# Kernel tuning notes

Hardware: AMD Instinct MI355X
Metric: run time of the kernel (lower is better)

Reference implementation:

```python
import math
import jax, jax.numpy as jnp
import numpy as np

B, S, E, H = 4, 1024, 1024, 16
DH = E // H
LN_EPS = 1e-5


def _layernorm(x, g, b):
    mu = jnp.mean(x, axis=-1, keepdims=True)
    var = jnp.mean(jnp.square(x - mu), axis=-1, keepdims=True)
    return (x - mu) * jax.lax.rsqrt(var + LN_EPS) * g + b


def _gelu_tanh(x):
    c = math.sqrt(2.0 / math.pi)
    return 0.5 * x * (1.0 + jnp.tanh(c * (x + 0.044715 * x * x * x)))


def setup_inputs() -> dict:
    key = jax.random.key(0)
    ks = jax.random.split(key, 12)
    std = 0.02
    x = jax.random.normal(ks[0], (B, S, E), jnp.float32)
    # additive causal mask: 0 on/below diag, -inf above
    causal_mask = jnp.where(jnp.tril(jnp.ones((S, S), bool)), 0.0, -jnp.inf).astype(jnp.float32)
    inp = dict(
        x=x,
        causal_mask=causal_mask,
        ln1_g=1.0 + std * jax.random.normal(ks[1], (E,), jnp.float32),
        ln1_b=std * jax.random.normal(ks[2], (E,), jnp.float32),
        ln2_g=1.0 + std * jax.random.normal(ks[3], (E,), jnp.float32),
        ln2_b=std * jax.random.normal(ks[4], (E,), jnp.float32),
        w_in=std * jax.random.normal(ks[5], (3 * E, E), jnp.float32),   # packed QKV in_proj_weight
        b_in=jnp.zeros((3 * E,), jnp.float32),
        w_out=std * jax.random.normal(ks[6], (E, E), jnp.float32),      # out_proj.weight
        b_out=jnp.zeros((E,), jnp.float32),
        w_fc=std * jax.random.normal(ks[7], (4 * E, E), jnp.float32),
        b_fc=jnp.zeros((4 * E,), jnp.float32),
        w_proj=std * jax.random.normal(ks[8], (E, 4 * E), jnp.float32),
        b_proj=jnp.zeros((E,), jnp.float32),
    )
    return inp


def reference(x, causal_mask, ln1_g, ln1_b, ln2_g, ln2_b,
              w_in, b_in, w_out, b_out, w_fc, b_fc, w_proj, b_proj):
    # --- attention branch (pre-LN) ---
    h = _layernorm(x, ln1_g, ln1_b)                       # [B,S,E]
    wq, wk, wv = w_in[:E], w_in[E:2 * E], w_in[2 * E:]
    bq, bk, bv = b_in[:E], b_in[E:2 * E], b_in[2 * E:]
    q = (h @ wq.T + bq).reshape(B, S, H, DH)
    k = (h @ wk.T + bk).reshape(B, S, H, DH)
    v = (h @ wv.T + bv).reshape(B, S, H, DH)
    scale = 1.0 / math.sqrt(DH)
    scores = jnp.einsum('bqhd,bkhd->bhqk', q * scale, k) + causal_mask  # [B,H,S,S]
    probs = jax.nn.softmax(scores, axis=-1)
    att = jnp.einsum('bhqk,bkhd->bqhd', probs, v).reshape(B, S, E)
    att = att @ w_out.T + b_out
    att_weights = jnp.mean(probs, axis=1)                 # averaged over heads, [B,S,S]
    x = x + att
    # --- MLP branch (pre-LN) ---
    h2 = _layernorm(x, ln2_g, ln2_b)
    x = x + (_gelu_tanh(h2 @ w_fc.T + b_fc) @ w_proj.T + b_proj)
    return (x, att_weights)
```

## Files before the change

kernel.cpp:

```cpp
#include <hip/hip_runtime.h>

typedef unsigned short u16;
typedef u16   u16x4 __attribute__((ext_vector_type(4)));
typedef u16   u16x8 __attribute__((ext_vector_type(8)));
typedef short s16x8 __attribute__((ext_vector_type(8)));
typedef float f32x4 __attribute__((ext_vector_type(4)));

__device__ __forceinline__ float b2f(u16 u) {
    union { unsigned int i; float f; } v; v.i = ((unsigned int)u) << 16; return v.f;
}
__device__ __forceinline__ u16 f2b(float f) {
    union { float f; unsigned int i; } v; v.f = f;
    unsigned int r = v.i + 0x7fffu + ((v.i >> 16) & 1u);
    return (u16)(r >> 16);
}
__device__ __forceinline__ float gelu_f(float x) {
    float z = 0.7978845608028654f * (x + 0.044715f * x * x * x);
    float e = __expf(2.0f * z);
    float t = 1.0f - 2.0f / (e + 1.0f);
    return 0.5f * x * (1.0f + t);
}
__device__ __forceinline__ void async16(const u16* g, u16* l) {
    __builtin_amdgcn_global_load_lds(
        (const __attribute__((address_space(1))) unsigned int*)g,
        (__attribute__((address_space(3))) unsigned int*)l,
        16, 0, 0);
}

#define FEN() asm volatile("" ::: "memory")
#define BARR() { FEN(); __builtin_amdgcn_s_barrier(); FEN(); }
#define VMC(N) asm volatile("s_waitcnt vmcnt(" #N ")" ::: "memory")

__global__ __launch_bounds__(256)
void detect_k(const u16* __restrict__ x, int* __restrict__ flag)
{
    int gid = blockIdx.x * 256 + threadIdx.x;
    const u16x8 u = *(const u16x8*)(x + (long)gid * 8);
    int bad = 0;
    #pragma unroll
    for (int e = 0; e < 8; e++) {
        int ex = (u[e] >> 7) & 0xFF;
        if (ex >= 187) bad = 1;
    }
    unsigned long long m = __ballot(bad != 0);
    if ((threadIdx.x & 63) == 0 && m != 0ull) atomicOr(flag, 1);
}

__global__ __launch_bounds__(256)
void conv_w_k(const void* __restrict__ s0, const void* __restrict__ s1,
              const void* __restrict__ s2, const void* __restrict__ s3,
              u16* __restrict__ dst, const int* __restrict__ flag)
{
    const long MEG = 1L << 20;
    long gid = ((long)blockIdx.x * 256 + threadIdx.x) * 4;
    const void* s; long off;
    if      (gid <  3*MEG) { s = s0; off = gid; }
    else if (gid <  4*MEG) { s = s1; off = gid - 3*MEG; }
    else if (gid <  8*MEG) { s = s2; off = gid - 4*MEG; }
    else                   { s = s3; off = gid - 8*MEG; }
    u16x4 o;
    if (*flag) {
        const float4 f = *(const float4*)((const float*)s + off);
        o[0] = f2b(f.x); o[1] = f2b(f.y); o[2] = f2b(f.z); o[3] = f2b(f.w);
    } else {
        o = *(const u16x4*)((const u16*)s + off);
    }
    *(u16x4*)(dst + gid) = o;
}

__global__ __launch_bounds__(256)
void conv_small_k(const void* s0, const void* s1, const void* s2, const void* s3,
                  const void* s4, const void* s5, const void* s6, const void* s7,
                  u16* __restrict__ dst, const int* __restrict__ flag)
{
    int gid = blockIdx.x * 256 + threadIdx.x;
    int seg, off;
    if      (gid <  4096) { seg = gid >> 10;  off = gid & 1023; }
    else if (gid <  7168) { seg = 4; off = gid - 4096; }
    else if (gid <  8192) { seg = 5; off = gid - 7168; }
    else if (gid < 12288) { seg = 6; off = gid - 8192; }
    else                  { seg = 7; off = gid - 12288; }
    const void* srcs[8] = {s0, s1, s2, s3, s4, s5, s6, s7};
    const void* s = srcs[seg];
    dst[seg * 4096 + off] = (*flag) ? f2b(((const float*)s)[off]) : ((const u16*)s)[off];
}

__global__ __launch_bounds__(256)
void ln1x_k(const void* __restrict__ xraw, const u16* __restrict__ g,
            const u16* __restrict__ b, u16* __restrict__ xc,
            u16* __restrict__ o, const int* __restrict__ flag)
{
    long row = blockIdx.x;
    int tid = threadIdx.x;
    float v0, v1, v2, v3;
    if (*flag) {
        const float4 f = *(const float4*)((const float*)xraw + row * 1024 + tid * 4);
        v0 = b2f(f2b(f.x)); v1 = b2f(f2b(f.y));
        v2 = b2f(f2b(f.z)); v3 = b2f(f2b(f.w));
    } else {
        const u16x4 u = *(const u16x4*)((const u16*)xraw + row * 1024 + tid * 4);
        v0 = b2f(u[0]); v1 = b2f(u[1]); v2 = b2f(u[2]); v3 = b2f(u[3]);
    }
    u16x4 xv; xv[0] = f2b(v0); xv[1] = f2b(v1); xv[2] = f2b(v2); xv[3] = f2b(v3);
    *(u16x4*)(xc + row * 1024 + tid * 4) = xv;
    float s  = v0 + v1 + v2 + v3;
    float sq = v0*v0 + v1*v1 + v2*v2 + v3*v3;
    #pragma unroll
    for (int off = 32; off; off >>= 1) { s += __shfl_xor(s, off); sq += __shfl_xor(sq, off); }
    __shared__ float sm[8];
    int wid = tid >> 6, lane = tid & 63;
    if (lane == 0) { sm[wid] = s; sm[wid + 4] = sq; }
    __syncthreads();
    s  = sm[0] + sm[1] + sm[2] + sm[3];
    sq = sm[4] + sm[5] + sm[6] + sm[7];
    float mean = s * (1.0f / 1024.0f);
    float var  = sq * (1.0f / 1024.0f) - mean * mean;
    float rs   = rsqrtf(var + 1e-5f);
    u16x4 gg = *(const u16x4*)(g + tid * 4);
    u16x4 bb = *(const u16x4*)(b + tid * 4);
    u16x4 ov;
    ov[0] = f2b((v0 - mean) * rs * b2f(gg[0]) + b2f(bb[0]));
    ov[1] = f2b((v1 - mean) * rs * b2f(gg[1]) + b2f(bb[1]));
    ov[2] = f2b((v2 - mean) * rs * b2f(gg[2]) + b2f(bb[2]));
    ov[3] = f2b((v3 - mean) * rs * b2f(gg[3]) + b2f(bb[3]));
    *(u16x4*)(o + row * 1024 + tid * 4) = ov;
}

__global__ __launch_bounds__(256)
void ln_k(const u16* __restrict__ x, const u16* __restrict__ g,
          const u16* __restrict__ b, u16* __restrict__ o)
{
    long row = blockIdx.x;
    int tid = threadIdx.x;
    const u16x4 u = *(const u16x4*)(x + row * 1024 + tid * 4);
    float v0 = b2f(u[0]), v1 = b2f(u[1]), v2 = b2f(u[2]), v3 = b2f(u[3]);
    float s  = v0 + v1 + v2 + v3;
    float sq = v0*v0 + v1*v1 + v2*v2 + v3*v3;
    #pragma unroll
    for (int off = 32; off; off >>= 1) { s += __shfl_xor(s, off); sq += __shfl_xor(sq, off); }
    __shared__ float sm[8];
    int wid = tid >> 6, lane = tid & 63;
    if (lane == 0) { sm[wid] = s; sm[wid + 4] = sq; }
    __syncthreads();
    s  = sm[0] + sm[1] + sm[2] + sm[3];
    sq = sm[4] + sm[5] + sm[6] + sm[7];
    float mean = s * (1.0f / 1024.0f);
    float var  = sq * (1.0f / 1024.0f) - mean * mean;
    float rs   = rsqrtf(var + 1e-5f);
    u16x4 gg = *(const u16x4*)(g + tid * 4);
    u16x4 bb = *(const u16x4*)(b + tid * 4);
    u16x4 ov;
    ov[0] = f2b((v0 - mean) * rs * b2f(gg[0]) + b2f(bb[0]));
    ov[1] = f2b((v1 - mean) * rs * b2f(gg[1]) + b2f(bb[1]));
    ov[2] = f2b((v2 - mean) * rs * b2f(gg[2]) + b2f(bb[2]));
    ov[3] = f2b((v3 - mean) * rs * b2f(gg[3]) + b2f(bb[3]));
    *(u16x4*)(o + row * 1024 + tid * 4) = ov;
}

__global__ __launch_bounds__(256)
void redln_k(const float* __restrict__ P, long slice,
             const u16* __restrict__ bias, u16* __restrict__ res,
             const u16* __restrict__ g, const u16* __restrict__ b,
             u16* __restrict__ o)
{
    long row = blockIdx.x;
    int tid = threadIdx.x;
    long i = row * 1024 + tid * 4;
    float4 v  = *(const float4*)(P + i);
    float4 p1 = *(const float4*)(P + slice + i);
    u16x4 bb = *(const u16x4*)(bias + tid * 4);
    u16x4 rr = *(const u16x4*)(res + i);
    float v0 = b2f(f2b(v.x + p1.x + b2f(bb[0]) + b2f(rr[0])));
    float v1 = b2f(f2b(v.y + p1.y + b2f(bb[1]) + b2f(rr[1])));
    float v2 = b2f(f2b(v.z + p1.z + b2f(bb[2]) + b2f(rr[2])));
    float v3 = b2f(f2b(v.w + p1.w + b2f(bb[3]) + b2f(rr[3])));
    u16x4 xv; xv[0] = f2b(v0); xv[1] = f2b(v1); xv[2] = f2b(v2); xv[3] = f2b(v3);
    *(u16x4*)(res + i) = xv;
    float s  = v0 + v1 + v2 + v3;
    float sq = v0*v0 + v1*v1 + v2*v2 + v3*v3;
    #pragma unroll
    for (int off = 32; off; off >>= 1) { s += __shfl_xor(s, off); sq += __shfl_xor(sq, off); }
    __shared__ float sm[8];
    int wid = tid >> 6, lane = tid & 63;
    if (lane == 0) { sm[wid] = s; sm[wid + 4] = sq; }
    __syncthreads();
    s  = sm[0] + sm[1] + sm[2] + sm[3];
    sq = sm[4] + sm[5] + sm[6] + sm[7];
    float mean = s * (1.0f / 1024.0f);
    float var  = sq * (1.0f / 1024.0f) - mean * mean;
    float rs   = rsqrtf(var + 1e-5f);
    u16x4 gg = *(const u16x4*)(g + tid * 4);
    u16x4 b2 = *(const u16x4*)(b + tid * 4);
    u16x4 ov;
    ov[0] = f2b((v0 - mean) * rs * b2f(gg[0]) + b2f(b2[0]));
    ov[1] = f2b((v1 - mean) * rs * b2f(gg[1]) + b2f(b2[1]));
    ov[2] = f2b((v2 - mean) * rs * b2f(gg[2]) + b2f(b2[2]));
    ov[3] = f2b((v3 - mean) * rs * b2f(gg[3]) + b2f(b2[3]));
    *(u16x4*)(o + row * 1024 + tid * 4) = ov;
}

__global__ __launch_bounds__(1024)
void smmean_k(u16* __restrict__ probs, void* __restrict__ ow, long ofs,
              const int* __restrict__ flag)
{
    const long MEG = 1L << 20;
    __shared__ float red[16 * 1024];
    int bl = blockIdx.x >> 10;
    int q  = blockIdx.x & 1023;
    int w = threadIdx.x >> 6, lane = threadIdx.x & 63;
    int tile_end = ((q >> 7) + 1) << 7;
    u16* row = probs + (((long)(bl * 16 + w)) << 20) + (long)q * 1024;
    float v[16];
    float m = -3.0e38f;
    #pragma unroll
    for (int c = 0; c < 2; c++) {
        int kb = (c * 64 + lane) * 8;
        if (kb <= q) {
            u16x8 u = *(const u16x8*)(row + kb);
            #pragma unroll
            for (int e = 0; e < 8; e++) {
                if (kb + e <= q) {
                    float f = b2f(u[e]);
                    v[c * 8 + e] = f;
                    m = fmaxf(m, f);
                } else v[c * 8 + e] = -3.0e38f;
            }
        } else {
            #pragma unroll
            for (int e = 0; e < 8; e++) v[c * 8 + e] = -3.0e38f;
        }
    }
    #pragma unroll
    for (int off = 32; off; off >>= 1) m = fmaxf(m, __shfl_xor(m, off));
    float s = 0.0f;
    #pragma unroll
    for (int t = 0; t < 16; t++) {
        float e = (v[t] > -1.0e38f) ? __expf(v[t] - m) : 0.0f;
        v[t] = e; s += e;
    }
    #pragma unroll
    for (int off = 32; off; off >>= 1) s += __shfl_xor(s, off);
    float inv = 1.0f / s;
    #pragma unroll
    for (int c = 0; c < 2; c++) {
        int kb = (c * 64 + lane) * 8;
        float p[8];
        #pragma unroll
        for (int e = 0; e < 8; e++) p[e] = v[c * 8 + e] * inv;
        #pragma unroll
        for (int e = 0; e < 8; e++) red[w * 1024 + kb + e] = p[e];
        if (kb < tile_end) {
            u16x8 o;
            #pragma unroll
            for (int e = 0; e < 8; e++) o[e] = f2b(p[e]);
            *(u16x8*)(row + kb) = o;
        }
    }
    __syncthreads();
    int t = threadIdx.x;
    float acc = 0.0f;
    #pragma unroll
    for (int h = 0; h < 16; h++) acc += red[h * 1024 + t];
    acc *= 0.0625f;
    long idx = ofs + (long)bl * MEG + (long)q * 1024 + t;
    if (*flag) ((float*)ow)[idx] = acc;
    else       ((u16*)ow)[idx]   = f2b(acc);
}

__global__ __launch_bounds__(256)
void reduce_out_k(const float* __restrict__ P, long slice,
                  const u16* __restrict__ bias, const u16* __restrict__ res,
                  void* __restrict__ out, const int* __restrict__ flag)
{
    long i = ((long)blockIdx.x * 256 + threadIdx.x) * 4;
    int gn = (int)(i & 1023);
    float4 v = *(const float4*)(P + i);
    #pragma unroll
    for (int s = 1; s < 4; s++) {
        const float4 p = *(const float4*)(P + (long)s * slice + i);
        v.x += p.x; v.y += p.y; v.z += p.z; v.w += p.w;
    }
    u16x4 bb = *(const u16x4*)(bias + gn);
    u16x4 rr = *(const u16x4*)(res + i);
    v.x += b2f(bb[0]) + b2f(rr[0]);
    v.y += b2f(bb[1]) + b2f(rr[1]);
    v.z += b2f(bb[2]) + b2f(rr[2]);
    v.w += b2f(bb[3]) + b2f(rr[3]);
    if (*flag) {
        *(float4*)((float*)out + i) = v;
    } else {
        u16x4 o;
        o[0] = f2b(v.x); o[1] = f2b(v.y); o[2] = f2b(v.z); o[3] = f2b(v.w);
        *(u16x4*)((u16*)out + i) = o;
    }
}

template<int EPI>
__global__ __launch_bounds__(512, 2)
void g8(const u16* __restrict__ A, const u16* __restrict__ Bt,
        u16* __restrict__ C, const u16* __restrict__ bias,
        float* __restrict__ Cf,
        int K, int lda, int ldb, int ldc,
        long sA, long sB, long sC)
{
    __shared__ alignas(16) u16 shA[2 * 16384];
    __shared__ alignas(16) u16 shB[2 * 16384];

    const int tid = threadIdx.x;
    int tn = blockIdx.x, tm = blockIdx.y;
    const int bz = blockIdx.z;
    {
        int L = blockIdx.y * gridDim.x + blockIdx.x;
        int xcd = L & 7, idx = L >> 3;
        tn = idx % gridDim.x;
        tm = (idx / gridDim.x) * 8 + xcd;
    }
    const u16* Ab = A + (long)bz * sA;
    const u16* Bb = Bt + (long)bz * sB;
    const int m0 = tm * 256, n0 = tn * 256;
    const int NT = K >> 6;

    const int w = tid >> 6, lane = tid & 63;
    const int lr = lane & 15, quad = lane >> 4, sw = lane & 7;
    const int wm16 = (w >> 2) * 16, wn16 = (w & 3) * 16;

    auto stageH = [&](int tile, int isB, int half) {
        const u16* src = isB ? Bb : Ab;
        const int ld = isB ? ldb : lda;
        const int r0 = (isB ? n0 : m0) + half * 128;
        u16* dbase = (isB ? shB : shA) + (tile & 1) * 16384 + half * 8192;
        const long kk = (long)tile << 6;
        #pragma unroll
        for (int L2 = 0; L2 < 2; L2++) {
            int c = L2 * 512 + tid;
            int rl = c >> 3, sl = c & 7;
            int kc = sl ^ (rl & 7);
            async16(src + (long)(r0 + rl) * ld + kk + kc * 8, dbase + c * 8);
        }
    };

    f32x4 acc[2][4][2][2] = {};
    s16x8 aF[4][2], b0F[2][2], b1F[2][2];

    auto rdA = [&](int buf, int ih) {
        #pragma unroll
        for (int q = 0; q < 4; q++)
            #pragma unroll
            for (int ks = 0; ks < 2; ks++)
                aF[q][ks] = *(const s16x8*)&shA[buf * 16384 + ih * 8192
                    + (q * 32 + wm16 + lr) * 64 + ((ks * 4 + quad) ^ sw) * 8];
    };
    auto rdB = [&](s16x8 (&bF)[2][2], int buf, int jh) {
        #pragma unroll
        for (int r = 0; r < 2; r++)
            #pragma unroll
            for (int ks = 0; ks < 2; ks++)
                bF[r][ks] = *(const s16x8*)&shB[buf * 16384 + jh * 8192
                    + (r * 64 + wn16 + lr) * 64 + ((ks * 4 + quad) ^ sw) * 8];
    };

#define MM(IH, JH, BF) do { \
    __builtin_amdgcn_s_setprio(1); \
    _Pragma("unroll") \
    for (int q = 0; q < 4; q++) \
        _Pragma("unroll") \
        for (int r = 0; r < 2; r++) \
            _Pragma("unroll") \
            for (int ks = 0; ks < 2; ks++) \
                acc[IH][q][JH][r] = __builtin_amdgcn_mfma_f32_16x16x32_bf16( \
                    aF[q][ks], BF[r][ks], acc[IH][q][JH][r], 0, 0, 0); \
    __builtin_amdgcn_s_setprio(0); \
} while (0)

    stageH(0, 0, 0); stageH(0, 1, 0); stageH(0, 1, 1);
    stageH(1, 0, 0); stageH(1, 1, 0); stageH(0, 0, 1);
    VMC(8); BARR();

    for (int t = 0; t < NT - 2; ++t) {
        const int buf = t & 1;
        rdA(buf, 0); rdB(b0F, buf, 0); stageH(t + 1, 1, 1);
        BARR(); MM(0, 0, b0F);
        FEN(); VMC(8); BARR();
        rdB(b1F, buf, 1); stageH(t + 2, 0, 0);
        BARR(); MM(0, 1, b1F);
        FEN(); VMC(4); BARR();
        rdA(buf, 1); stageH(t + 2, 1, 0);
        BARR(); MM(1, 0, b0F);
        BARR();
        stageH(t + 1, 0, 1);
        BARR(); MM(1, 1, b1F);
        BARR();
    }

    {
        const int buf = (NT - 2) & 1;
        rdA(buf, 0); rdB(b0F, buf, 0); stageH(NT - 1, 1, 1);
        BARR(); MM(0, 0, b0F);
        FEN(); VMC(8); BARR();
        rdB(b1F, buf, 1);
        BARR(); MM(0, 1, b1F);
        FEN(); VMC(2); BARR();
        rdA(buf, 1);
        BARR(); MM(1, 0, b0F);
        BARR();
        stageH(NT - 1, 0, 1);
        BARR(); MM(1, 1, b1F);
        BARR();
    }
    {
        const int buf = (NT - 1) & 1;
        rdA(buf, 0); rdB(b0F, buf, 0);
        BARR(); MM(0, 0, b0F);
        FEN(); VMC(2); BARR();
        rdB(b1F, buf, 1);
        BARR(); MM(0, 1, b1F);
        FEN(); VMC(0); BARR();
        rdA(buf, 1);
        BARR(); MM(1, 0, b0F);
        BARR();
        MM(1, 1, b1F);
    }
#undef MM

    #pragma unroll
    for (int ih = 0; ih < 2; ih++)
        #pragma unroll
        for (int q = 0; q < 4; q++)
            #pragma unroll
            for (int jh = 0; jh < 2; jh++)
                #pragma unroll
                for (int r = 0; r < 2; r++)
                    #pragma unroll
                    for (int rr = 0; rr < 4; rr++) {
                        int gm = m0 + ih * 128 + q * 32 + wm16 + quad * 4 + rr;
                        int gn = n0 + jh * 128 + r * 64 + wn16 + lr;
                        float v = acc[ih][q][jh][r][rr];
                        if (EPI == 3) {
                            C[(long)gm * ldc + gn] = f2b(gelu_f(v + b2f(bias[gn])));
                        } else {
                            Cf[(long)bz * sC + (long)gm * ldc + gn] = v;
                        }
                    }
}

template<int BN, int EPI>
__global__ __launch_bounds__(256)
void gemm_bt(const u16* __restrict__ A, const u16* __restrict__ Bt,
             u16* __restrict__ C, const u16* __restrict__ bias,
             const u16* __restrict__ res,
             u16* __restrict__ qb, u16* __restrict__ kb, u16* __restrict__ vb,
             int M, int N, int K, int lda, int ldb, int ldc,
             long sA, long sB, long sC,
             const int* __restrict__ oflag, void* __restrict__ oout)
{
    constexpr int BM = 128, BK = 32;
    constexpr int WROWS = (BN == 128) ? 2 : 4;
    constexpr int WCOLS = (BN == 128) ? 2 : 1;
    constexpr int WM = BM / WROWS, WN = BN / WCOLS;
    constexpr int MI = WM / 16, NJ = WN / 16;
    constexpr int BCH = BN * BK / 8 / 256;
    constexpr int SHSZ = 2 * BM * BK + 2 * BN * BK;

    __shared__ alignas(16) u16 shmem[SHSZ];
    u16* AshB = shmem;
    u16* BshB = shmem + 2 * BM * BK;
    u16* Csh  = shmem;

    const int tid = threadIdx.x;
    int tn = blockIdx.x, tm = blockIdx.y;
    const int bz = blockIdx.z;
    if (EPI == 4 && tn > tm) return;

    if (EPI == 1 || EPI == 2 || EPI == 3 || EPI == 6 || EPI == 7) {
        int L = blockIdx.y * gridDim.x + blockIdx.x;
        int xcd = L & 7, idx = L >> 3;
        tn = idx % gridDim.x;
        tm = (idx / gridDim.x) * 8 + xcd;
    }

    const u16* Ab = A + (long)bz * sA;
    const u16* Bb = Bt + (long)bz * sB;

    const int m0 = tm * BM, n0 = tn * BN;
    const int kEff = (EPI == 5) ? (((tm + 1) * BM < K) ? (tm + 1) * BM : K) : K;

    const int w = tid >> 6, lane = tid & 63;
    const int wrow = w % WROWS, wcol = w / WROWS;
    const int mw = wrow * WM, nw = wcol * WN;
    const int lr = lane & 15, quad = lane >> 4;

    const int ca0 = tid, ca1 = 256 + tid;
    const int cb1 = 256 + tid;

    const int ar0 = ca0 >> 2, ac0 = (((ca0 & 3) ^ ((ca0 >> 3) & 3))) * 8;
    const int ar1 = ca1 >> 2, ac1 = (((ca1 & 3) ^ ((ca1 >> 3) & 3))) * 8;
    const int br0 = tid >> 2, bc0 = (((tid & 3) ^ ((tid >> 3) & 3))) * 8;
    const int br1 = cb1 >> 2, bc1 = (((cb1 & 3) ^ ((cb1 >> 3) & 3))) * 8;

    auto stage = [&](int buf, int k0) {
        async16(Ab + (long)(m0 + ar0) * lda + k0 + ac0, &AshB[buf * BM * BK + ca0 * 8]);
        async16(Ab + (long)(m0 + ar1) * lda + k0 + ac1, &AshB[buf * BM * BK + ca1 * 8]);
        async16(Bb + (long)(n0 + br0) * ldb + k0 + bc0, &BshB[buf * BN * BK + tid * 8]);
        if (BCH == 2)
            async16(Bb + (long)(n0 + br1) * ldb + k0 + bc1, &BshB[buf * BN * BK + cb1 * 8]);
    };

    f32x4 acc[MI][NJ] = {};

    const int foff = (quad ^ ((lr >> 1) & 3)) * 8;

    stage(0, 0);
    int cur = 0;
    for (int k0 = 0; k0 < kEff; k0 += BK) {
        __syncthreads();
        if (k0 + BK < kEff) stage(cur ^ 1, k0 + BK);

        s16x8 af[MI], bfr[NJ];
        #pragma unroll
        for (int i = 0; i < MI; i++)
            af[i] = *(const s16x8*)&AshB[cur * BM * BK + (mw + i * 16 + lr) * BK + foff];
        #pragma unroll
        for (int j = 0; j < NJ; j++)
            bfr[j] = *(const s16x8*)&BshB[cur * BN * BK + (nw + j * 16 + lr) * BK + foff];
        #pragma unroll
        for (int i = 0; i < MI; i++)
            #pragma unroll
            for (int j = 0; j < NJ; j++)
                acc[i][j] = __builtin_amdgcn_mfma_f32_16x16x32_bf16(af[i], bfr[j], acc[i][j], 0, 0, 0);
        cur ^= 1;
    }

    if (EPI == 1) {
        const int sel = n0 >> 10;
        const int b = m0 >> 10, sbase = m0 & 1023;
        if (sel < 2) {
            u16* dst = (sel == 0) ? qb : kb;
            #pragma unroll
            for (int i = 0; i < MI; i++)
                #pragma unroll
                for (int j = 0; j < NJ; j++)
                    #pragma unroll
                    for (int r = 0; r < 4; r++) {
                        int gm = m0 + mw + i * 16 + quad * 4 + r;
                        int gn = n0 + nw + j * 16 + lr;
                        float v = acc[i][j][r] + b2f(bias[gn]);
                        int s = gm & 1023, nn = gn & 1023, hh = nn >> 6, d = nn & 63;
                        dst[(((long)(b * 16 + hh) * 1024 + s) << 6) + d] = f2b(v);
                    }
        } else {
            __syncthreads();
            #pragma unroll
            for (int i = 0; i < MI; i++)
                #pragma unroll
                for (int j = 0; j < NJ; j++)
                    #pragma unroll
                    for (int r = 0; r < 4; r++) {
                        int nl = nw + j * 16 + lr;
                        int ml = mw + i * 16 + quad * 4 + r;
                        float v = acc[i][j][r] + b2f(bias[n0 + nl]);
                        Csh[nl * 128 + (((ml >> 3) ^ (nl & 15)) << 3) + (ml & 7)] = f2b(v);
                    }
            __syncthreads();
            const int nv0 = n0 - 2048;
            #pragma unroll
            for (int rep = 0; rep < 8; rep++) {
                int dd = rep * 16 + (tid >> 4);
                int sl = (tid & 15) * 8;
                int dg = nv0 + dd, hh = dg >> 6, dcol = dg & 63;
                u16x8 val = *(const u16x8*)&Csh[dd * 128 + ((((sl >> 3)) ^ (dd & 15)) << 3)];
                *(u16x8*)&vb[(((long)(b * 16 + hh) * 64 + dcol) << 10) + sbase + sl] = val;
            }
        }
        return;
    }

    u16* Cb;
    if (EPI == 5) Cb = C + (long)(bz >> 4) * (1 << 20) + (bz & 15) * 64;
    else          Cb = C + (long)bz * sC;

    #pragma unroll
    for (int i = 0; i < MI; i++) {
        #pragma unroll
        for (int j = 0; j < NJ; j++) {
            #pragma unroll
            for (int r = 0; r < 4; r++) {
                int gm = m0 + mw + i * 16 + quad * 4 + r;
                int gn = n0 + nw + j * 16 + lr;
                float v = acc[i][j][r];
                if (EPI == 5) {
                    Cb[(long)gm * ldc + gn] = f2b(v);
                } else if (EPI == 2) {
                    v += b2f(bias[gn]) + b2f(res[(long)gm * ldc + gn]);
                    Cb[(long)gm * ldc + gn] = f2b(v);
                } else if (EPI == 3) {
                    Cb[(long)gm * ldc + gn] = f2b(gelu_f(v + b2f(bias[gn])));
                } else if (EPI == 4) {
                    if (gn <= gm) Cb[(long)gm * ldc + gn] = f2b(v * 0.125f);
                } else if (EPI == 6) {
                    v += b2f(bias[gn]) + b2f(res[(long)gm * ldc + gn]);
                    long idx = (long)gm * ldc + gn;
                    if (*oflag) ((float*)oout)[idx] = v;
                    else        ((u16*)oout)[idx]   = f2b(v);
                } else if (EPI == 7) {
                    ((float*)oout)[(long)bz * sC + (long)gm * ldc + gn] = v;
                }
            }
        }
    }
}

extern "C" void kernel_launch(void* const* d_in, const int* in_sizes, int n_in,
                              void* d_out, int out_size, void* d_ws, size_t ws_size,
                              hipStream_t stream)
{
    const long MEG = 1L << 20;
    const long KI  = 1024;

    u16* ws = (u16*)d_ws;
    u16* xc    = ws;
    u16* winC  = ws + 4  * MEG;
    u16* woutC = ws + 7  * MEG;
    u16* wfcC  = ws + 8  * MEG;
    u16* wprjC = ws + 12 * MEG;
    u16* sm    = ws + 16 * MEG;
    u16* ln1g = sm + 0*4*KI, *ln1b = sm + 1*4*KI;
    u16* ln2g = sm + 2*4*KI, *ln2b = sm + 3*4*KI;
    u16* binC = sm + 4*4*KI;
    u16* boutC= sm + 5*4*KI;
    u16* bfcC = sm + 6*4*KI;
    u16* bprjC= sm + 7*4*KI;
    int* flag = (int*)(sm + 8*4*KI);
    u16* slotA = ws + 16 * MEG + 64 * KI;
    u16* qB    = slotA + 4  * MEG;
    u16* kB    = slotA + 8  * MEG;
    u16* vT    = slotA + 12 * MEG;
    u16* probs = slotA + 16 * MEG;
    float* part = (float*)(probs + 16 * MEG);

    const long fixed_elems = 32 * MEG + 64 * KI;
    const long avail = (long)(ws_size / 2);
    int chunk = 1;
    if      (avail >= fixed_elems + 64 * MEG) chunk = 4;
    else if (avail >= fixed_elems + 32 * MEG) chunk = 2;
    const bool splitk = (chunk == 4);

    hipMemsetAsync((void*)flag, 0, sizeof(int), stream);
    detect_k<<<32, 256, 0, stream>>>((const u16*)d_in[0], flag);
    conv_w_k<<<12288, 256, 0, stream>>>(d_in[6], d_in[8], d_in[10], d_in[12],
                                        winC, flag);
    conv_small_k<<<52, 256, 0, stream>>>(d_in[2], d_in[3], d_in[4], d_in[5],
                                         d_in[7], d_in[9], d_in[11], d_in[13],
                                         sm, flag);

    u16* h   = slotA;
    u16* att = slotA;
    u16* h2  = slotA;
    u16* act = probs;

    ln1x_k<<<4096, 256, 0, stream>>>(d_in[0], ln1g, ln1b, xc, h, flag);
    gemm_bt<128, 1><<<dim3(24, 32, 1), 256, 0, stream>>>(
        h, winC, nullptr, binC, nullptr, qB, kB, vT,
        4096, 3072, 1024, 1024, 1024, 0, 0, 0, 0, nullptr, nullptr);
    for (int b0 = 0; b0 < 4; b0 += chunk) {
        gemm_bt<128, 4><<<dim3(8, 8, 16 * chunk), 256, 0, stream>>>(
            qB + b0 * MEG, kB + b0 * MEG, probs, nullptr, nullptr,
            nullptr, nullptr, nullptr,
            1024, 1024, 64, 64, 64, 1024, 65536, 65536, 1048576, nullptr, nullptr);
        smmean_k<<<1024 * chunk, 1024, 0, stream>>>(probs, d_out,
                                                    4 * MEG + b0 * MEG, flag);
        gemm_bt<64, 5><<<dim3(1, 8, 16 * chunk), 256, 0, stream>>>(
            probs, vT + b0 * MEG, att + b0 * MEG, nullptr, nullptr,
            nullptr, nullptr, nullptr,
            1024, 64, 1024, 1024, 1024, 1024, 1048576, 65536, 0, nullptr, nullptr);
    }
    if (splitk) {
        g8<7><<<dim3(4, 16, 2), 512, 0, stream>>>(
            att, woutC, nullptr, nullptr, part,
            512, 1024, 1024, 1024, 512, 512, 4 * MEG);
        redln_k<<<4096, 256, 0, stream>>>(part, 4 * MEG, boutC, xc, ln2g, ln2b, h2);
    } else {
        gemm_bt<128, 2><<<dim3(8, 32, 1), 256, 0, stream>>>(
            att, woutC, xc, boutC, xc, nullptr, nullptr, nullptr,
            4096, 1024, 1024, 1024, 1024, 1024, 0, 0, 0, nullptr, nullptr);
        ln_k<<<4096, 256, 0, stream>>>(xc, ln2g, ln2b, h2);
    }
    g8<3><<<dim3(16, 16, 1), 512, 0, stream>>>(
        h2, wfcC, act, bfcC, nullptr,
        1024, 1024, 1024, 4096, 0, 0, 0);
    if (splitk) {
        g8<7><<<dim3(4, 16, 4), 512, 0, stream>>>(
            act, wprjC, nullptr, nullptr, part,
            1024, 4096, 4096, 1024, 1024, 1024, 4 * MEG);
        reduce_out_k<<<4096, 256, 0, stream>>>(part, 4 * MEG, bprjC, xc, d_out, flag);
    } else {
        gemm_bt<128, 6><<<dim3(8, 32, 1), 256, 0, stream>>>(
            act, wprjC, nullptr, bprjC, xc, nullptr, nullptr, nullptr,
            4096, 1024, 4096, 4096, 4096, 1024, 0, 0, 0, flag, d_out);
    }
}
```

Measured before the change: 409.8 us.

## Split out-proj GEMM into 4 K-slices and drop pre-MFMA barriers in g8

The attention output projection's split-K factor goes from 2 to 4 (K=256 per slice), and the reduce+LayerNorm kernel now sums four partial slices, so more workgroups are in flight. Separately, the g8 GEMM main loop drops the barrier between each LDS fragment read and the MFMA block that follows. The barriers around staging are kept. Removing those barriers cuts synchronisation stalls, but it relies on the remaining barriers and waits to keep the double-buffered LDS reads ordered against the async stores. The extra split-K also adds partial-sum traffic to the reduction.

```diff
diff --git a/kernel.cpp b/kernel.cpp
--- a/kernel.cpp
+++ b/kernel.cpp
@@ -168,12 +168,18 @@
     long i = row * 1024 + tid * 4;
     float4 v  = *(const float4*)(P + i);
     float4 p1 = *(const float4*)(P + slice + i);
+    float4 p2 = *(const float4*)(P + 2 * slice + i);
+    float4 p3 = *(const float4*)(P + 3 * slice + i);
+    v.x += p1.x + p2.x + p3.x;
+    v.y += p1.y + p2.y + p3.y;
+    v.z += p1.z + p2.z + p3.z;
+    v.w += p1.w + p2.w + p3.w;
     u16x4 bb = *(const u16x4*)(bias + tid * 4);
     u16x4 rr = *(const u16x4*)(res + i);
-    float v0 = b2f(f2b(v.x + p1.x + b2f(bb[0]) + b2f(rr[0])));
-    float v1 = b2f(f2b(v.y + p1.y + b2f(bb[1]) + b2f(rr[1])));
-    float v2 = b2f(f2b(v.z + p1.z + b2f(bb[2]) + b2f(rr[2])));
-    float v3 = b2f(f2b(v.w + p1.w + b2f(bb[3]) + b2f(rr[3])));
+    float v0 = b2f(f2b(v.x + b2f(bb[0]) + b2f(rr[0])));
+    float v1 = b2f(f2b(v.y + b2f(bb[1]) + b2f(rr[1])));
+    float v2 = b2f(f2b(v.z + b2f(bb[2]) + b2f(rr[2])));
+    float v3 = b2f(f2b(v.w + b2f(bb[3]) + b2f(rr[3])));
     u16x4 xv; xv[0] = f2b(v0); xv[1] = f2b(v1); xv[2] = f2b(v2); xv[3] = f2b(v3);
     *(u16x4*)(res + i) = xv;
     float s  = v0 + v1 + v2 + v3;
@@ -379,44 +385,44 @@
     for (int t = 0; t < NT - 2; ++t) {
         const int buf = t & 1;
         rdA(buf, 0); rdB(b0F, buf, 0); stageH(t + 1, 1, 1);
-        BARR(); MM(0, 0, b0F);
+        MM(0, 0, b0F);
         FEN(); VMC(8); BARR();
         rdB(b1F, buf, 1); stageH(t + 2, 0, 0);
-        BARR(); MM(0, 1, b1F);
+        MM(0, 1, b1F);
         FEN(); VMC(4); BARR();
         rdA(buf, 1); stageH(t + 2, 1, 0);
-        BARR(); MM(1, 0, b0F);
+        MM(1, 0, b0F);
         BARR();
         stageH(t + 1, 0, 1);
-        BARR(); MM(1, 1, b1F);
+        MM(1, 1, b1F);
         BARR();
     }
 
     {
         const int buf = (NT - 2) & 1;
         rdA(buf, 0); rdB(b0F, buf, 0); stageH(NT - 1, 1, 1);
-        BARR(); MM(0, 0, b0F);
+        MM(0, 0, b0F);
         FEN(); VMC(8); BARR();
         rdB(b1F, buf, 1);
-        BARR(); MM(0, 1, b1F);
+        MM(0, 1, b1F);
         FEN(); VMC(2); BARR();
         rdA(buf, 1);
-        BARR(); MM(1, 0, b0F);
+        MM(1, 0, b0F);
         BARR();
         stageH(NT - 1, 0, 1);
-        BARR(); MM(1, 1, b1F);
+        MM(1, 1, b1F);
         BARR();
     }
     {
         const int buf = (NT - 1) & 1;
         rdA(buf, 0); rdB(b0F, buf, 0);
-        BARR(); MM(0, 0, b0F);
+        MM(0, 0, b0F);
         FEN(); VMC(2); BARR();
         rdB(b1F, buf, 1);
-        BARR(); MM(0, 1, b1F);
+        MM(0, 1, b1F);
         FEN(); VMC(0); BARR();
         rdA(buf, 1);
-        BARR(); MM(1, 0, b0F);
+        MM(1, 0, b0F);
         BARR();
         MM(1, 1, b1F);
     }
@@ -674,9 +680,9 @@
             1024, 64, 1024, 1024, 1024, 1024, 1048576, 65536, 0, nullptr, nullptr);
     }
     if (splitk) {
-        g8<7><<<dim3(4, 16, 2), 512, 0, stream>>>(
+        g8<7><<<dim3(4, 16, 4), 512, 0, stream>>>(
             att, woutC, nullptr, nullptr, part,
-            512, 1024, 1024, 1024, 512, 512, 4 * MEG);
+            256, 1024, 1024, 1024, 256, 256, 4 * MEG);
         redln_k<<<4096, 256, 0, stream>>>(part, 4 * MEG, boutC, xc, ln2g, ln2b, h2);
     } else {
         gemm_bt<128, 2><<<dim3(8, 32, 1), 256, 0, stream>>>(
```

Measured after the change: 420.8 us. 1.03x slower.

## Double-buffer register fragments to overlap LDS reads with MFMA in GEMM loop

Applied to the files above, without the earlier changes.

Restructures the 256x256 GEMM main loop to unroll by two K tiles. It keeps separate A and B register fragment sets (A0/A1, B0e/B0o/B1) so LDS reads for the next quadrant are issued before the current MFMA block. It also reorders the global-to-LDS staging and drops some barriers. The goal is to hide LDS read latency behind matrix math and cut barrier stalls, at the cost of higher VGPR pressure and a more fragile synchronisation schedule that assumes an even tile count.

```diff
diff --git a/kernel.cpp b/kernel.cpp
--- a/kernel.cpp
+++ b/kernel.cpp
@@ -340,26 +340,24 @@
     };
 
     f32x4 acc[2][4][2][2] = {};
-    s16x8 aF[4][2], b0F[2][2], b1F[2][2];
-
-    auto rdA = [&](int buf, int ih) {
+    s16x8 A0[4][2], A1[4][2], B0e[2][2], B0o[2][2], B1[2][2];
+
+    auto rdAh = [&](s16x8 (&dst)[4][2], int buf, int ih, int ks) {
         #pragma unroll
         for (int q = 0; q < 4; q++)
+            dst[q][ks] = *(const s16x8*)&shA[buf * 16384 + ih * 8192
+                + (q * 32 + wm16 + lr) * 64 + ((ks * 4 + quad) ^ sw) * 8];
+    };
+    auto rdBf = [&](s16x8 (&dst)[2][2], int buf, int jh) {
+        #pragma unroll
+        for (int r = 0; r < 2; r++)
             #pragma unroll
             for (int ks = 0; ks < 2; ks++)
-                aF[q][ks] = *(const s16x8*)&shA[buf * 16384 + ih * 8192
-                    + (q * 32 + wm16 + lr) * 64 + ((ks * 4 + quad) ^ sw) * 8];
-    };
-    auto rdB = [&](s16x8 (&bF)[2][2], int buf, int jh) {
-        #pragma unroll
-        for (int r = 0; r < 2; r++)
-            #pragma unroll
-            for (int ks = 0; ks < 2; ks++)
-                bF[r][ks] = *(const s16x8*)&shB[buf * 16384 + jh * 8192
+                dst[r][ks] = *(const s16x8*)&shB[buf * 16384 + jh * 8192
                     + (r * 64 + wn16 + lr) * 64 + ((ks * 4 + quad) ^ sw) * 8];
     };
 
-#define MM(IH, JH, BF) do { \
+#define MM(IH, JH, AF, BF) do { \
     __builtin_amdgcn_s_setprio(1); \
     _Pragma("unroll") \
     for (int q = 0; q < 4; q++) \
@@ -368,58 +366,63 @@
             _Pragma("unroll") \
             for (int ks = 0; ks < 2; ks++) \
                 acc[IH][q][JH][r] = __builtin_amdgcn_mfma_f32_16x16x32_bf16( \
-                    aF[q][ks], BF[r][ks], acc[IH][q][JH][r], 0, 0, 0); \
+                    AF[q][ks], BF[r][ks], acc[IH][q][JH][r], 0, 0, 0); \
     __builtin_amdgcn_s_setprio(0); \
 } while (0)
 
-    stageH(0, 0, 0); stageH(0, 1, 0); stageH(0, 1, 1);
-    stageH(1, 0, 0); stageH(1, 1, 0); stageH(0, 0, 1);
-    VMC(8); BARR();
-
-    for (int t = 0; t < NT - 2; ++t) {
-        const int buf = t & 1;
-        rdA(buf, 0); rdB(b0F, buf, 0); stageH(t + 1, 1, 1);
-        BARR(); MM(0, 0, b0F);
-        FEN(); VMC(8); BARR();
-        rdB(b1F, buf, 1); stageH(t + 2, 0, 0);
-        BARR(); MM(0, 1, b1F);
+    stageH(0, 0, 0); stageH(0, 1, 0); stageH(0, 0, 1); stageH(0, 1, 1);
+    stageH(1, 0, 0); stageH(1, 1, 0);
+    VMC(4); BARR();
+    rdAh(A0, 0, 0, 0); rdAh(A0, 0, 0, 1); rdBf(B0e, 0, 0);
+
+    for (int t = 0; t < NT - 2; t += 2) {
+        rdBf(B1, 0, 1); rdAh(A1, 0, 1, 0); stageH(t + 1, 0, 1);
+        MM(0, 0, A0, B0e);
+        BARR();
+        rdAh(A1, 0, 1, 1); stageH(t + 1, 1, 1);
+        MM(0, 1, A0, B1);
         FEN(); VMC(4); BARR();
-        rdA(buf, 1); stageH(t + 2, 1, 0);
-        BARR(); MM(1, 0, b0F);
+        rdBf(B0o, 1, 0); rdAh(A0, 1, 0, 0); stageH(t + 2, 0, 0);
+        MM(1, 0, A1, B0e);
         BARR();
-        stageH(t + 1, 0, 1);
-        BARR(); MM(1, 1, b1F);
+        rdAh(A0, 1, 0, 1); stageH(t + 2, 1, 0);
+        MM(1, 1, A1, B1);
+        FEN(); VMC(4); BARR();
+        rdBf(B1, 1, 1); rdAh(A1, 1, 1, 0); stageH(t + 2, 0, 1);
+        MM(0, 0, A0, B0o);
         BARR();
-    }
-
-    {
-        const int buf = (NT - 2) & 1;
-        rdA(buf, 0); rdB(b0F, buf, 0); stageH(NT - 1, 1, 1);
-        BARR(); MM(0, 0, b0F);
-        FEN(); VMC(8); BARR();
-        rdB(b1F, buf, 1);
-        BARR(); MM(0, 1, b1F);
-        FEN(); VMC(2); BARR();
-        rdA(buf, 1);
-        BARR(); MM(1, 0, b0F);
+        rdAh(A1, 1, 1, 1); stageH(t + 2, 1, 1);
+        MM(0, 1, A0, B1);
+        FEN(); VMC(4); BARR();
+        rdBf(B0e, 0, 0); rdAh(A0, 0, 0, 0); stageH(t + 3, 0, 0);
+        MM(1, 0, A1, B0o);
         BARR();
-        stageH(NT - 1, 0, 1);
-        BARR(); MM(1, 1, b1F);
-        BARR();
-    }
-    {
-        const int buf = (NT - 1) & 1;
-        rdA(buf, 0); rdB(b0F, buf, 0);
-        BARR(); MM(0, 0, b0F);
-        FEN(); VMC(2); BARR();
-        rdB(b1F, buf, 1);
-        BARR(); MM(0, 1, b1F);
-        FEN(); VMC(0); BARR();
-        rdA(buf, 1);
-        BARR(); MM(1, 0, b0F);
-        BARR();
-        MM(1, 1, b1F);
-    }
+        rdAh(A0, 0, 0, 1); stageH(t + 3, 1, 0);
+        MM(1, 1, A1, B1);
+        FEN(); VMC(4); BARR();
+    }
+
+    rdBf(B1, 0, 1); rdAh(A1, 0, 1, 0); stageH(NT - 1, 0, 1);
+    MM(0, 0, A0, B0e);
+    BARR();
+    rdAh(A1, 0, 1, 1); stageH(NT - 1, 1, 1);
+    MM(0, 1, A0, B1);
+    FEN(); VMC(4); BARR();
+    rdBf(B0o, 1, 0); rdAh(A0, 1, 0, 0);
+    MM(1, 0, A1, B0e);
+    BARR();
+    rdAh(A0, 1, 0, 1);
+    MM(1, 1, A1, B1);
+    FEN(); VMC(0); BARR();
+    rdBf(B1, 1, 1); rdAh(A1, 1, 1, 0);
+    MM(0, 0, A0, B0o);
+    BARR();
+    rdAh(A1, 1, 1, 1);
+    MM(0, 1, A0, B1);
+    BARR();
+    MM(1, 0, A1, B0o);
+    BARR();
+    MM(1, 1, A1, B1);
 #undef MM
 
     #pragma unroll
```

Result: slower. 526.8 us (+28.5%).
